# Kernel tuning notes

Hardware: AMD Instinct MI355X
Metric: run time of the kernel (lower is better)

## Reference

```python
import jax, jax.numpy as jnp
import numpy as np

EMBED_DIM = 1024
N_HEADS = 16
HEAD_DIM = EMBED_DIM // N_HEADS


def setup_inputs() -> dict:
    key = jax.random.key(0)
    ks = jax.random.split(key, 11)
    B, S = 4, 2048
    s = 0.02
    return {
        "queries": jax.random.normal(ks[0], (B, S, EMBED_DIM), dtype=jnp.float32),
        "keys": jax.random.normal(ks[1], (B, S, EMBED_DIM), dtype=jnp.float32),
        "values": jax.random.normal(ks[2], (B, S, EMBED_DIM), dtype=jnp.float32),
        "W_q": jax.random.normal(ks[3], (HEAD_DIM, HEAD_DIM), dtype=jnp.float32) * s,
        "b_q": jax.random.normal(ks[4], (HEAD_DIM,), dtype=jnp.float32) * s,
        "W_k": jax.random.normal(ks[5], (HEAD_DIM, HEAD_DIM), dtype=jnp.float32) * s,
        "b_k": jax.random.normal(ks[6], (HEAD_DIM,), dtype=jnp.float32) * s,
        "W_v": jax.random.normal(ks[7], (HEAD_DIM, HEAD_DIM), dtype=jnp.float32) * s,
        "b_v": jax.random.normal(ks[8], (HEAD_DIM,), dtype=jnp.float32) * s,
        "W_p": jax.random.normal(ks[9], (EMBED_DIM, EMBED_DIM), dtype=jnp.float32) * s,
        "b_p": jax.random.normal(ks[10], (EMBED_DIM,), dtype=jnp.float32) * s,
    }


def reference(queries, keys, values, W_q, b_q, W_k, b_k, W_v, b_v, W_p, b_p):
    B, S, _ = queries.shape
    scale = HEAD_DIM ** 0.5  # module uses head_dim ** (1/2)
    # split heads: [B, S, H, hd]
    q = queries.reshape(B, S, N_HEADS, HEAD_DIM)
    k = keys.reshape(B, S, N_HEADS, HEAD_DIM)
    v = values.reshape(B, S, N_HEADS, HEAD_DIM)
    # per-head projections (weights shared across heads); torch Linear: x @ W.T + b
    q = jnp.einsum('bshd,ed->bhse', q, W_q) + b_q
    k = jnp.einsum('bshd,ed->bhse', k, W_k) + b_k
    v = jnp.einsum('bshd,ed->bhse', v, W_v) + b_v
    # scaled dot-product attention
    scores = jnp.einsum('bhqd,bhkd->bhqk', q, k) / scale  # [B,H,S,S]
    attn = jax.nn.softmax(scores, axis=-1)
    ctx = jnp.einsum('bhqk,bhkd->bhqd', attn, v)  # [B,H,S,hd]
    # merge heads and final projection
    ctx = ctx.transpose(0, 2, 1, 3).reshape(B, S, EMBED_DIM)
    return ctx @ W_p.T + b_p
```

## Files before the change

kernel.cpp:

```cpp
#include <hip/hip_runtime.h>
#include <hip/hip_bf16.h>

#define EMBED 1024
#define NH 16
#define HD 64
#define BSZ 4
#define SSZ 2048
#define LSTR 72

typedef __attribute__((ext_vector_type(8))) short short8;
typedef __attribute__((ext_vector_type(4))) short short4v;
typedef __attribute__((ext_vector_type(4))) float float4v;
typedef __attribute__((ext_vector_type(2))) unsigned int uint2v;

__device__ inline float4v mfma16(short8 a, short8 b, float4v c) {
    return __builtin_amdgcn_mfma_f32_16x16x32_bf16(a, b, c, 0, 0, 0);
}

__device__ inline float fexp2(float x) { return __builtin_amdgcn_exp2f(x); }

__device__ inline short f2bf(float f) {
    unsigned u = __builtin_bit_cast(unsigned, f);
    return (short)((u + 0x8000u) >> 16);
}
__device__ inline unsigned pk2(float a, float b) {
    unsigned ua = __builtin_bit_cast(unsigned, a);
    unsigned ub = __builtin_bit_cast(unsigned, b);
    return ((ua + 0x8000u) >> 16) | (((ub + 0x8000u) >> 16) << 16);
}
__device__ inline short8 ld8_f32_bf16(const float* p) {
    float4v lo = *(const float4v*)p;
    float4v hi = *(const float4v*)(p + 4);
    short8 r;
#pragma unroll
    for (int i = 0; i < 4; ++i) { r[i] = f2bf(lo[i]); r[i + 4] = f2bf(hi[i]); }
    return r;
}

__device__ inline void glds16(const short* gsrc, short* ldst) {
    __builtin_amdgcn_global_load_lds(
        (const __attribute__((address_space(1))) unsigned int*)gsrc,
        (__attribute__((address_space(3))) unsigned int*)ldst,
        16, 0, 0);
}

__global__ __launch_bounds__(256) void wp_cvt_kernel(
    const float* __restrict__ Wp, short* __restrict__ Wpb)
{
    int i = (blockIdx.x * 256 + threadIdx.x) * 4;
    float4v v = *(const float4v*)(Wp + i);
    short4v s;
#pragma unroll
    for (int j = 0; j < 4; ++j) s[j] = f2bf(v[j]);
    *(short4v*)(Wpb + i) = s;
}

__global__ __launch_bounds__(256) void qkv_kernel(
    const float* __restrict__ q_in, const float* __restrict__ k_in,
    const float* __restrict__ v_in,
    const float* __restrict__ Wq, const float* __restrict__ bq,
    const float* __restrict__ Wk, const float* __restrict__ bk,
    const float* __restrict__ Wv, const float* __restrict__ bv,
    short* __restrict__ qp, short* __restrict__ kp, short* __restrict__ vt)
{
    __shared__ __align__(16) short Xb[64 * LSTR];
    __shared__ __align__(16) short Wb[64 * LSTR];

    int z = blockIdx.z;
    const float* X    = z == 0 ? q_in : (z == 1 ? k_in : v_in);
    const float* W    = z == 0 ? Wq   : (z == 1 ? Wk   : Wv);
    const float* bias = z == 0 ? bq   : (z == 1 ? bk   : bv);
    const float scale = z == 0 ? 0.125f * 1.44269504f : 1.0f;

    int tid = threadIdx.x;
    int wave = tid >> 6, lane = tid & 63, quad = lane >> 4, l16 = lane & 15;
    int h = blockIdx.y;
    int rbase = blockIdx.x * 64;
    int b = rbase >> 11;
    int sbase = rbase & (SSZ - 1);
    int bh = b * NH + h;

    int srow = tid >> 2, c16 = (tid & 3) * 16;
    {
        const float* xsrc = X + (size_t)(rbase + srow) * EMBED + h * HD + c16;
        short8 x0 = ld8_f32_bf16(xsrc);
        short8 x1 = ld8_f32_bf16(xsrc + 8);
        *(short8*)&Xb[srow * LSTR + c16] = x0;
        *(short8*)&Xb[srow * LSTR + c16 + 8] = x1;
        const float* wsrc = W + (size_t)srow * HD + c16;
        short8 w0 = ld8_f32_bf16(wsrc);
        short8 w1 = ld8_f32_bf16(wsrc + 8);
        *(short8*)&Wb[srow * LSTR + c16] = w0;
        *(short8*)&Wb[srow * LSTR + c16 + 8] = w1;
    }
    __syncthreads();

    short8 a0 = *(const short8*)&Xb[(wave * 16 + l16) * LSTR + quad * 8];
    short8 a1 = *(const short8*)&Xb[(wave * 16 + l16) * LSTR + 32 + quad * 8];
    float4v acc[4];
#pragma unroll
    for (int nt = 0; nt < 4; ++nt) acc[nt] = (float4v)(0.f);
#pragma unroll
    for (int nt = 0; nt < 4; ++nt) {
        short8 b0 = *(const short8*)&Wb[(nt * 16 + l16) * LSTR + quad * 8];
        short8 b1 = *(const short8*)&Wb[(nt * 16 + l16) * LSTR + 32 + quad * 8];
        acc[nt] = mfma16(a0, b0, acc[nt]);
        acc[nt] = mfma16(a1, b1, acc[nt]);
    }
    __syncthreads();

    if (z < 2) {
#pragma unroll
        for (int nt = 0; nt < 4; ++nt) {
            float bv_ = bias[nt * 16 + l16];
#pragma unroll
            for (int r = 0; r < 4; ++r) {
                float val = (acc[nt][r] + bv_) * scale;
                Xb[(wave * 16 + quad * 4 + r) * LSTR + nt * 16 + l16] = f2bf(val);
            }
        }
        __syncthreads();
        short8 r0 = *(const short8*)&Xb[srow * LSTR + c16];
        short8 r1 = *(const short8*)&Xb[srow * LSTR + c16 + 8];
        short* Y = z == 0 ? qp : kp;
        size_t o = ((size_t)bh * SSZ + sbase + srow) * HD + c16;
        *(short8*)&Y[o] = r0;
        *(short8*)&Y[o + 8] = r1;
    } else {
#pragma unroll
        for (int nt = 0; nt < 4; ++nt) {
            float bv_ = bias[nt * 16 + l16];
            uint2v p;
            p[0] = pk2(acc[nt][0] + bv_, acc[nt][1] + bv_);
            p[1] = pk2(acc[nt][2] + bv_, acc[nt][3] + bv_);
            *(uint2v*)&Xb[(nt * 16 + l16) * LSTR + wave * 16 + quad * 4] = p;
        }
        __syncthreads();
        short8 r0 = *(const short8*)&Xb[srow * LSTR + c16];
        short8 r1 = *(const short8*)&Xb[srow * LSTR + c16 + 8];
        size_t o = ((size_t)bh * HD + srow) * SSZ + sbase + c16;
        *(short8*)&vt[o] = r0;
        *(short8*)&vt[o + 8] = r1;
    }
}

__global__ __launch_bounds__(512, 4) void attn_kernel(
    const short* __restrict__ qp, const short* __restrict__ kp,
    const short* __restrict__ vt, short* __restrict__ ctx)
{
    __shared__ __align__(16) short Kls[64 * LSTR];
    __shared__ __align__(16) short Vls[64 * LSTR];
    __shared__ __align__(16) short Pl[8 * 32 * LSTR];

    int tid = threadIdx.x;
    int wave = tid >> 6, lane = tid & 63, quad = lane >> 4, l16 = lane & 15;
    int bh = blockIdx.x;
    int b = bh >> 4, h = bh & 15;
    int qrow0 = blockIdx.y * 256 + wave * 32;

    const short* Qb = qp + (size_t)bh * SSZ * HD;
    const short* Kb = kp + (size_t)bh * SSZ * HD;
    const short* Vb = vt + (size_t)bh * HD * SSZ;

    int srow = tid >> 3;
    int scol = (tid & 7) * 8;
    const short* ksrc = Kb + srow * HD + scol;
    const short* vsrc = Vb + (size_t)srow * SSZ + scol;
    short* kdst = &Kls[srow * LSTR + scol];
    short* vdst = &Vls[srow * LSTR + scol];

    short8 qf[2][2];
#pragma unroll
    for (int nt = 0; nt < 2; ++nt)
#pragma unroll
        for (int c = 0; c < 2; ++c)
            qf[nt][c] = *(const short8*)&Qb[(size_t)(qrow0 + nt * 16 + l16) * HD + c * 32 + quad * 8];

    const short one = (short)0x3F80;
    short8 ones = {one, one, one, one, one, one, one, one};

    float4v oacc[4][2];
#pragma unroll
    for (int dt = 0; dt < 4; ++dt)
#pragma unroll
        for (int nt = 0; nt < 2; ++nt) oacc[dt][nt] = (float4v)(0.f);
    float4v lacc[2];
    lacc[0] = (float4v)(0.f); lacc[1] = (float4v)(0.f);

    short* Pw = Pl + wave * 32 * LSTR;

    {
        short8 kr = *(const short8*)(ksrc);
        short8 vr = *(const short8*)(vsrc);
        *(short8*)kdst = kr;
        *(short8*)vdst = vr;
    }
    __syncthreads();

    for (int kt = 0; kt < SSZ / 64; ++kt) {
        short8 krn, vrn;
        if (kt < 31) {
            krn = *(const short8*)(ksrc + (kt + 1) * 64 * HD);
            vrn = *(const short8*)(vsrc + (kt + 1) * 64);
        }
        float4v sacc[4][2];
#pragma unroll
        for (int mt = 0; mt < 4; ++mt) {
            sacc[mt][0] = (float4v)(0.f); sacc[mt][1] = (float4v)(0.f);
        }
#pragma unroll
        for (int mt = 0; mt < 4; ++mt)
#pragma unroll
            for (int c = 0; c < 2; ++c) {
                short8 kf = *(const short8*)&Kls[(mt * 16 + l16) * LSTR + c * 32 + quad * 8];
                sacc[mt][0] = mfma16(kf, qf[0][c], sacc[mt][0]);
                sacc[mt][1] = mfma16(kf, qf[1][c], sacc[mt][1]);
            }
#pragma unroll
        for (int mt = 0; mt < 4; ++mt)
#pragma unroll
            for (int nt = 0; nt < 2; ++nt) {
                float e0 = fexp2(sacc[mt][nt][0]);
                float e1 = fexp2(sacc[mt][nt][1]);
                float e2 = fexp2(sacc[mt][nt][2]);
                float e3 = fexp2(sacc[mt][nt][3]);
                uint2v p; p[0] = pk2(e0, e1); p[1] = pk2(e2, e3);
                *(uint2v*)&Pw[(nt * 16 + l16) * LSTR + mt * 16 + quad * 4] = p;
            }
        short8 pf[2][2];
#pragma unroll
        for (int nt = 0; nt < 2; ++nt)
#pragma unroll
            for (int c = 0; c < 2; ++c)
                pf[nt][c] = *(const short8*)&Pw[(nt * 16 + l16) * LSTR + c * 32 + quad * 8];
#pragma unroll
        for (int nt = 0; nt < 2; ++nt)
#pragma unroll
            for (int c = 0; c < 2; ++c)
                lacc[nt] = mfma16(ones, pf[nt][c], lacc[nt]);
#pragma unroll
        for (int dt = 0; dt < 4; ++dt)
#pragma unroll
            for (int c = 0; c < 2; ++c) {
                short8 vf = *(const short8*)&Vls[(dt * 16 + l16) * LSTR + c * 32 + quad * 8];
                oacc[dt][0] = mfma16(vf, pf[0][c], oacc[dt][0]);
                oacc[dt][1] = mfma16(vf, pf[1][c], oacc[dt][1]);
            }
        __syncthreads();
        if (kt < 31) {
            *(short8*)kdst = krn;
            *(short8*)vdst = vrn;
        }
        __syncthreads();
    }
    float rl[2];
    rl[0] = 1.0f / lacc[0][0];
    rl[1] = 1.0f / lacc[1][0];
#pragma unroll
    for (int dt = 0; dt < 4; ++dt)
#pragma unroll
        for (int nt = 0; nt < 2; ++nt) {
            uint2v p;
            p[0] = pk2(oacc[dt][nt][0] * rl[nt], oacc[dt][nt][1] * rl[nt]);
            p[1] = pk2(oacc[dt][nt][2] * rl[nt], oacc[dt][nt][3] * rl[nt]);
            size_t o = ((size_t)(b * SSZ + qrow0 + nt * 16 + l16)) * EMBED
                       + h * HD + dt * 16 + quad * 4;
            *(uint2v*)&ctx[o] = p;
        }
}

__global__ __launch_bounds__(256) void proj_kernel(
    const short* __restrict__ ctx, const short* __restrict__ Wpb,
    const float* __restrict__ bp, float* __restrict__ out)
{
    __shared__ __align__(16) short Als[128 * 64];
    __shared__ __align__(16) short Bls[128 * 64];

    int tid = threadIdx.x;
    int wave = tid >> 6, lane = tid & 63, quad = lane >> 4, l16 = lane & 15;
    int wm = wave >> 1, wn = wave & 1;
    int row0 = blockIdx.x * 128;
    int col0 = blockIdx.y * 128;

    int lrow = lane >> 3;
    int lcol = (lane & 7) * 8;
    const short* ag = ctx + (size_t)(row0 + wave * 32 + lrow) * EMBED + lcol;
    const short* bg = Wpb + (size_t)(col0 + wave * 32 + lrow) * EMBED + lcol;

    float4v acc[4][4];
#pragma unroll
    for (int mt = 0; mt < 4; ++mt)
#pragma unroll
        for (int nt = 0; nt < 4; ++nt) acc[mt][nt] = (float4v)(0.f);

    for (int kc = 0; kc < EMBED / 64; ++kc) {
#pragma unroll
        for (int i = 0; i < 4; ++i) {
            glds16(ag + (size_t)(i * 8) * EMBED + kc * 64,
                   &Als[(wave * 32 + i * 8) * 64]);
            glds16(bg + (size_t)(i * 8) * EMBED + kc * 64,
                   &Bls[(wave * 32 + i * 8) * 64]);
        }
        __syncthreads();
#pragma unroll
        for (int ks = 0; ks < 2; ++ks) {
            short8 af[4], bf[4];
#pragma unroll
            for (int mt = 0; mt < 4; ++mt)
                af[mt] = *(const short8*)&Als[(wm * 64 + mt * 16 + l16) * 64 + ks * 32 + quad * 8];
#pragma unroll
            for (int nt = 0; nt < 4; ++nt)
                bf[nt] = *(const short8*)&Bls[(wn * 64 + nt * 16 + l16) * 64 + ks * 32 + quad * 8];
#pragma unroll
            for (int mt = 0; mt < 4; ++mt)
#pragma unroll
                for (int nt = 0; nt < 4; ++nt)
                    acc[mt][nt] = mfma16(af[mt], bf[nt], acc[mt][nt]);
        }
        __syncthreads();
    }
#pragma unroll
    for (int nt = 0; nt < 4; ++nt) {
        float bias = bp[col0 + wn * 64 + nt * 16 + l16];
#pragma unroll
        for (int mt = 0; mt < 4; ++mt)
#pragma unroll
            for (int r = 0; r < 4; ++r) {
                int row = row0 + wm * 64 + mt * 16 + quad * 4 + r;
                out[(size_t)row * EMBED + col0 + wn * 64 + nt * 16 + l16] = acc[mt][nt][r] + bias;
            }
    }
}

extern "C" void kernel_launch(void* const* d_in, const int* in_sizes, int n_in,
                              void* d_out, int out_size, void* d_ws, size_t ws_size,
                              hipStream_t stream) {
    const float* q_in = (const float*)d_in[0];
    const float* k_in = (const float*)d_in[1];
    const float* v_in = (const float*)d_in[2];
    const float* Wq   = (const float*)d_in[3];
    const float* bq   = (const float*)d_in[4];
    const float* Wk   = (const float*)d_in[5];
    const float* bk   = (const float*)d_in[6];
    const float* Wv   = (const float*)d_in[7];
    const float* bv   = (const float*)d_in[8];
    const float* Wp   = (const float*)d_in[9];
    const float* bp   = (const float*)d_in[10];

    const size_t TENS = (size_t)BSZ * SSZ * EMBED;
    short* ws  = (short*)d_ws;
    short* qp  = ws;
    short* kp  = qp + TENS;
    short* vtp = kp + TENS;
    short* ctx = vtp + TENS;
    short* wpb = ctx + TENS;

    wp_cvt_kernel<<<dim3(EMBED * EMBED / 1024), 256, 0, stream>>>(Wp, wpb);
    qkv_kernel<<<dim3(BSZ * SSZ / 64, NH, 3), 256, 0, stream>>>(
        q_in, k_in, v_in, Wq, bq, Wk, bk, Wv, bv, qp, kp, vtp);
    attn_kernel<<<dim3(BSZ * NH, SSZ / 256), 512, 0, stream>>>(qp, kp, vtp, ctx);
    proj_kernel<<<dim3(BSZ * SSZ / 128, EMBED / 128), 256, 0, stream>>>(
        ctx, wpb, bp, (float*)d_out);
}
```

Before: 277.1 us.

## Rewrite attention inner loop with 32x32 MFMA and register-resident P via permlane swap

Switches the attention kernel from 16x16x32 to 32x32x16 bf16 MFMAs and stores K/V in LDS in a pre-swizzled fragment layout. The exponentiated scores are packed with v_cvt_pk_bf16_f32 and rearranged with v_permlane32_swap so they feed the PV MFMA straight from registers, removing the per-wave P round trip through LDS. The aim is to cut LDS traffic and conversion instructions. In exchange it relies on gfx950-specific inline asm and writes ctx with scalar 2-byte stores instead of packed vector stores.

Result: no change. 272.3 us (-1.7%).

```diff
diff --git a/kernel.cpp b/kernel.cpp
--- a/kernel.cpp
+++ b/kernel.cpp
@@ -11,10 +11,15 @@
 typedef __attribute__((ext_vector_type(8))) short short8;
 typedef __attribute__((ext_vector_type(4))) short short4v;
 typedef __attribute__((ext_vector_type(4))) float float4v;
+typedef __attribute__((ext_vector_type(16))) float float16v;
 typedef __attribute__((ext_vector_type(2))) unsigned int uint2v;
+typedef __attribute__((ext_vector_type(4))) unsigned int uint4v;
 
 __device__ inline float4v mfma16(short8 a, short8 b, float4v c) {
     return __builtin_amdgcn_mfma_f32_16x16x32_bf16(a, b, c, 0, 0, 0);
+}
+__device__ inline float16v mfma32(short8 a, short8 b, float16v c) {
+    return __builtin_amdgcn_mfma_f32_32x32x16_bf16(a, b, c, 0, 0, 0);
 }
 
 __device__ inline float fexp2(float x) { return __builtin_amdgcn_exp2f(x); }
@@ -27,6 +32,11 @@
     unsigned ua = __builtin_bit_cast(unsigned, a);
     unsigned ub = __builtin_bit_cast(unsigned, b);
     return ((ua + 0x8000u) >> 16) | (((ub + 0x8000u) >> 16) << 16);
+}
+__device__ inline unsigned cvtpk(float a, float b) {
+    unsigned r;
+    asm("v_cvt_pk_bf16_f32 %0, %1, %2" : "=v"(r) : "v"(a), "v"(b));
+    return r;
 }
 __device__ inline short8 ld8_f32_bf16(const float* p) {
     float4v lo = *(const float4v*)p;
@@ -148,12 +158,12 @@
     const short* __restrict__ qp, const short* __restrict__ kp,
     const short* __restrict__ vt, short* __restrict__ ctx)
 {
-    __shared__ __align__(16) short Kls[64 * LSTR];
-    __shared__ __align__(16) short Vls[64 * LSTR];
-    __shared__ __align__(16) short Pl[8 * 32 * LSTR];
+    __shared__ __align__(16) short Kfr[16 * 32 * 8];
+    __shared__ __align__(16) short Vfr[16 * 32 * 8];
 
     int tid = threadIdx.x;
-    int wave = tid >> 6, lane = tid & 63, quad = lane >> 4, l16 = lane & 15;
+    int wave = tid >> 6, lane = tid & 63;
+    int hi = lane >> 5, l31 = lane & 31;
     int bh = blockIdx.x;
     int b = bh >> 4, h = bh & 15;
     int qrow0 = blockIdx.y * 256 + wave * 32;
@@ -162,36 +172,32 @@
     const short* Kb = kp + (size_t)bh * SSZ * HD;
     const short* Vb = vt + (size_t)bh * HD * SSZ;
 
-    int srow = tid >> 3;
-    int scol = (tid & 7) * 8;
-    const short* ksrc = Kb + srow * HD + scol;
-    const short* vsrc = Vb + (size_t)srow * SSZ + scol;
-    short* kdst = &Kls[srow * LSTR + scol];
-    short* vdst = &Vls[srow * LSTR + scol];
-
-    short8 qf[2][2];
-#pragma unroll
-    for (int nt = 0; nt < 2; ++nt)
-#pragma unroll
-        for (int c = 0; c < 2; ++c)
-            qf[nt][c] = *(const short8*)&Qb[(size_t)(qrow0 + nt * 16 + l16) * HD + c * 32 + quad * 8];
+    int lrow = lane >> 3, pc = lane & 7;
+    int grow = wave * 8 + lrow;
+    const short* ksrc = Kb + (size_t)grow * HD + pc * 8;
+    const short* vsrc = Vb + (size_t)grow * SSZ + pc * 8;
+    int fidx = (((grow >> 5) * 8 + pc) * 32 + (grow & 31)) * 8;
+    short* kdst = &Kfr[fidx];
+    short* vdst = &Vfr[fidx];
+
+    short8 qf[4];
+#pragma unroll
+    for (int s = 0; s < 4; ++s)
+        qf[s] = *(const short8*)&Qb[(size_t)(qrow0 + l31) * HD + s * 16 + hi * 8];
+
+    const short* krd = &Kfr[(hi * 32 + l31) * 8];
+    const short* vrd = &Vfr[(hi * 32 + l31) * 8];
 
     const short one = (short)0x3F80;
     short8 ones = {one, one, one, one, one, one, one, one};
 
-    float4v oacc[4][2];
-#pragma unroll
-    for (int dt = 0; dt < 4; ++dt)
-#pragma unroll
-        for (int nt = 0; nt < 2; ++nt) oacc[dt][nt] = (float4v)(0.f);
-    float4v lacc[2];
-    lacc[0] = (float4v)(0.f); lacc[1] = (float4v)(0.f);
-
-    short* Pw = Pl + wave * 32 * LSTR;
+    float16v oacc0 = (float16v)(0.f);
+    float16v oacc1 = (float16v)(0.f);
+    float16v lacc  = (float16v)(0.f);
 
     {
-        short8 kr = *(const short8*)(ksrc);
-        short8 vr = *(const short8*)(vsrc);
+        short8 kr = *(const short8*)ksrc;
+        short8 vr = *(const short8*)vsrc;
         *(short8*)kdst = kr;
         *(short8*)vdst = vr;
     }
@@ -199,73 +205,54 @@
 
     for (int kt = 0; kt < SSZ / 64; ++kt) {
         short8 krn, vrn;
-        if (kt < 31) {
-            krn = *(const short8*)(ksrc + (kt + 1) * 64 * HD);
-            vrn = *(const short8*)(vsrc + (kt + 1) * 64);
-        }
-        float4v sacc[4][2];
-#pragma unroll
-        for (int mt = 0; mt < 4; ++mt) {
-            sacc[mt][0] = (float4v)(0.f); sacc[mt][1] = (float4v)(0.f);
-        }
-#pragma unroll
-        for (int mt = 0; mt < 4; ++mt)
-#pragma unroll
-            for (int c = 0; c < 2; ++c) {
-                short8 kf = *(const short8*)&Kls[(mt * 16 + l16) * LSTR + c * 32 + quad * 8];
-                sacc[mt][0] = mfma16(kf, qf[0][c], sacc[mt][0]);
-                sacc[mt][1] = mfma16(kf, qf[1][c], sacc[mt][1]);
+        if (kt < SSZ / 64 - 1) {
+            krn = *(const short8*)(ksrc + (size_t)(kt + 1) * (64 * HD));
+            vrn = *(const short8*)(vsrc + (size_t)(kt + 1) * 64);
+        }
+#pragma unroll
+        for (int t = 0; t < 2; ++t) {
+            float16v sacc = (float16v)(0.f);
+#pragma unroll
+            for (int s = 0; s < 4; ++s) {
+                short8 kf = *(const short8*)(krd + (t * 8 + 2 * s) * 256);
+                sacc = mfma32(kf, qf[s], sacc);
             }
 #pragma unroll
-        for (int mt = 0; mt < 4; ++mt)
-#pragma unroll
-            for (int nt = 0; nt < 2; ++nt) {
-                float e0 = fexp2(sacc[mt][nt][0]);
-                float e1 = fexp2(sacc[mt][nt][1]);
-                float e2 = fexp2(sacc[mt][nt][2]);
-                float e3 = fexp2(sacc[mt][nt][3]);
-                uint2v p; p[0] = pk2(e0, e1); p[1] = pk2(e2, e3);
-                *(uint2v*)&Pw[(nt * 16 + l16) * LSTR + mt * 16 + quad * 4] = p;
+            for (int sr = 0; sr < 2; ++sr) {
+                unsigned x0 = cvtpk(fexp2(sacc[sr * 8 + 0]), fexp2(sacc[sr * 8 + 1]));
+                unsigned x1 = cvtpk(fexp2(sacc[sr * 8 + 2]), fexp2(sacc[sr * 8 + 3]));
+                unsigned y0 = cvtpk(fexp2(sacc[sr * 8 + 4]), fexp2(sacc[sr * 8 + 5]));
+                unsigned y1 = cvtpk(fexp2(sacc[sr * 8 + 6]), fexp2(sacc[sr * 8 + 7]));
+                asm("v_permlane32_swap_b32 %0, %1" : "+v"(x0), "+v"(y0));
+                asm("v_permlane32_swap_b32 %0, %1" : "+v"(x1), "+v"(y1));
+                uint4v wv; wv[0] = x0; wv[1] = x1; wv[2] = y0; wv[3] = y1;
+                short8 pa = __builtin_bit_cast(short8, wv);
+                int sa = t * 2 + sr;
+                short8 vf0 = *(const short8*)(vrd + (2 * sa) * 256);
+                short8 vf1 = *(const short8*)(vrd + (8 + 2 * sa) * 256);
+                oacc0 = mfma32(pa, vf0, oacc0);
+                oacc1 = mfma32(pa, vf1, oacc1);
+                lacc  = mfma32(pa, ones, lacc);
             }
-        short8 pf[2][2];
-#pragma unroll
-        for (int nt = 0; nt < 2; ++nt)
-#pragma unroll
-            for (int c = 0; c < 2; ++c)
-                pf[nt][c] = *(const short8*)&Pw[(nt * 16 + l16) * LSTR + c * 32 + quad * 8];
-#pragma unroll
-        for (int nt = 0; nt < 2; ++nt)
-#pragma unroll
-            for (int c = 0; c < 2; ++c)
-                lacc[nt] = mfma16(ones, pf[nt][c], lacc[nt]);
-#pragma unroll
-        for (int dt = 0; dt < 4; ++dt)
-#pragma unroll
-            for (int c = 0; c < 2; ++c) {
-                short8 vf = *(const short8*)&Vls[(dt * 16 + l16) * LSTR + c * 32 + quad * 8];
-                oacc[dt][0] = mfma16(vf, pf[0][c], oacc[dt][0]);
-                oacc[dt][1] = mfma16(vf, pf[1][c], oacc[dt][1]);
-            }
-        __syncthreads();
-        if (kt < 31) {
+        }
+        __syncthreads();
+        if (kt < SSZ / 64 - 1) {
             *(short8*)kdst = krn;
             *(short8*)vdst = vrn;
         }
         __syncthreads();
     }
-    float rl[2];
-    rl[0] = 1.0f / lacc[0][0];
-    rl[1] = 1.0f / lacc[1][0];
-#pragma unroll
-    for (int dt = 0; dt < 4; ++dt)
-#pragma unroll
-        for (int nt = 0; nt < 2; ++nt) {
-            uint2v p;
-            p[0] = pk2(oacc[dt][nt][0] * rl[nt], oacc[dt][nt][1] * rl[nt]);
-            p[1] = pk2(oacc[dt][nt][2] * rl[nt], oacc[dt][nt][3] * rl[nt]);
-            size_t o = ((size_t)(b * SSZ + qrow0 + nt * 16 + l16)) * EMBED
-                       + h * HD + dt * 16 + quad * 4;
-            *(uint2v*)&ctx[o] = p;
+
+#pragma unroll
+    for (int g = 0; g < 4; ++g)
+#pragma unroll
+        for (int e = 0; e < 4; ++e) {
+            int r = g * 4 + e;
+            float rl = 1.0f / lacc[r];
+            int q = qrow0 + g * 8 + 4 * hi + e;
+            size_t o = (size_t)(b * SSZ + q) * EMBED + h * HD + l31;
+            ctx[o]      = f2bf(oacc0[r] * rl);
+            ctx[o + 32] = f2bf(oacc1[r] * rl);
         }
 }
 
```
